# Performance work log

Measured on AMD Instinct MI355X. Metric: run time of the kernel, lower is better.

## Reference

```python
import jax, jax.numpy as jnp
import numpy as np

H = 16   # n_heads == n_I
D = 64   # d_q = d_k = d_v = d_r
DX = H * D
B, S = 4, 2048

def setup_inputs() -> dict:
    key = jax.random.key(0)
    ks = jax.random.split(key, 9)
    sc = 0.02
    return {
        "value": jax.random.normal(ks[0], (B, S, DX), jnp.float32),
        "key":   jax.random.normal(ks[1], (B, S, DX), jnp.float32),
        "query": jax.random.normal(ks[2], (B, S, DX), jnp.float32),
        "Wq_w": jax.random.normal(ks[3], (DX, DX), jnp.float32) * sc,
        "Wq_b": jnp.zeros((DX,), jnp.float32),
        "Wk_w": jax.random.normal(ks[4], (DX, DX), jnp.float32) * sc,
        "Wk_b": jnp.zeros((DX,), jnp.float32),
        "Wv_w": jax.random.normal(ks[5], (DX, DX), jnp.float32) * sc,
        "Wv_b": jnp.zeros((DX,), jnp.float32),
        "Wr_w": jax.random.normal(ks[6], (DX, DX), jnp.float32) * sc,
        "Wr_b": jnp.zeros((DX,), jnp.float32),
        "Wout_w": jax.random.normal(ks[7], (DX, DX), jnp.float32) * sc,
        "Wout_b": jnp.zeros((DX,), jnp.float32),
    }

def _heads(x, b, s):
    # [b, s, H*D] -> [b, H, s, D]
    return x.reshape(b, s, H, D).transpose(0, 2, 1, 3)

def reference(value, key, query, Wq_w, Wq_b, Wk_w, Wk_b, Wv_w, Wv_b,
              Wr_w, Wr_b, Wout_w, Wout_b):
    b, s, _ = query.shape
    # torch nn.Linear: y = x @ W.T + b
    Q = _heads(query @ Wq_w.T + Wq_b, b, s)   # [b,H,s,D]
    K = _heads(key   @ Wk_w.T + Wk_b, b, s)
    V = _heads(value @ Wv_w.T + Wv_b, b, s)
    R = _heads(query @ Wr_w.T + Wr_b, b, s)
    dot_scale = jnp.sqrt(jnp.float32(D))
    scores = jnp.einsum("bhid,bhjd->bhij", Q, K) / dot_scale  # [b,H,s,s]
    attn = jax.nn.softmax(scores, axis=-1)                    # dropout p=0
    out = jnp.einsum("bhij,bhjd->bhid", attn, V)              # [b,H,s,D]
    out = out * R                                             # R-gating
    out = out.transpose(0, 2, 1, 3).reshape(b, s, H * D)
    return out @ Wout_w.T + Wout_b
```

## Files before the change

kernel.cpp:

```cpp
#include <hip/hip_runtime.h>
#include <hip/hip_bf16.h>

typedef __bf16 bf16;
typedef __bf16 bf16x4 __attribute__((ext_vector_type(4)));
typedef __bf16 bf16x8 __attribute__((ext_vector_type(8)));
typedef float  f32x4  __attribute__((ext_vector_type(4)));

#define MFMA_16x16x32(a, b, c) __builtin_amdgcn_mfma_f32_16x16x32_bf16((a), (b), (c), 0, 0, 0)

typedef const void __attribute__((address_space(1))) gvoid;
typedef void __attribute__((address_space(3))) svoid;

__device__ __forceinline__ void async_copy16(const void* gptr, void* ldsptr) {
    __builtin_amdgcn_global_load_lds((gvoid*)gptr, (svoid*)ldsptr, 16, 0, 0);
}

__device__ __forceinline__ int swz8(int row, int quad) {
    return (quad ^ ((row >> 1) & 3)) * 8;
}

__global__ void cvt3_acts(const float* __restrict__ s0, const float* __restrict__ s1,
                          const float* __restrict__ s2,
                          bf16* __restrict__ d0, bf16* __restrict__ d1, bf16* __restrict__ d2)
{
    constexpr int N4SEG = 8192 * 1024 / 4;
    int i = blockIdx.x * blockDim.x + threadIdx.x;
    const int stride = gridDim.x * blockDim.x;
    for (; i < 3 * N4SEG; i += stride) {
        const int seg = i / N4SEG;
        const int j = i - seg * N4SEG;
        const float* s = seg == 0 ? s0 : (seg == 1 ? s1 : s2);
        bf16* d = seg == 0 ? d0 : (seg == 1 ? d1 : d2);
        float4 v = ((const float4*)s)[j];
        bf16x4 o = { (bf16)v.x, (bf16)v.y, (bf16)v.z, (bf16)v.w };
        ((bf16x4*)d)[j] = o;
    }
}

__global__ void cvt5_wts(const float* __restrict__ s0, const float* __restrict__ s1,
                         const float* __restrict__ s2, const float* __restrict__ s3,
                         const float* __restrict__ s4,
                         bf16* __restrict__ d0, bf16* __restrict__ d1, bf16* __restrict__ d2,
                         bf16* __restrict__ d3, bf16* __restrict__ d4)
{
    constexpr int N4SEG = 1024 * 1024 / 4;
    int i = blockIdx.x * blockDim.x + threadIdx.x;
    const int stride = gridDim.x * blockDim.x;
    for (; i < 5 * N4SEG; i += stride) {
        const int seg = i / N4SEG;
        const int j = i - seg * N4SEG;
        const float* s = seg == 0 ? s0 : seg == 1 ? s1 : seg == 2 ? s2 : seg == 3 ? s3 : s4;
        bf16* d = seg == 0 ? d0 : seg == 1 ? d1 : seg == 2 ? d2 : seg == 3 ? d3 : d4;
        float4 v = ((const float4*)s)[j];
        bf16x4 o = { (bf16)v.x, (bf16)v.y, (bf16)v.z, (bf16)v.w };
        ((bf16x4*)d)[j] = o;
    }
}

__global__ void proj_fused(const bf16* __restrict__ xq, const bf16* __restrict__ xk,
                           const bf16* __restrict__ xv, const bf16* __restrict__ wall,
                           const float* __restrict__ ball,
                           bf16* __restrict__ qr, bf16* __restrict__ kws,
                           bf16* __restrict__ vtws)
{
    constexpr int K = 1024, SDIM = 2048;
    __shared__ alignas(16) bf16 As[2][128 * 32];
    __shared__ alignas(16) bf16 Bs[2][128 * 32];

    const int tid  = threadIdx.x;
    const int lane = tid & 63;
    const int wave = tid >> 6;
    const int wm   = wave >> 1;
    const int wn   = wave & 1;
    const int bm   = blockIdx.x * 128;
    const int by   = blockIdx.y;
    const int bn   = by * 128;
    const int l15  = lane & 15;
    const int quad = lane >> 4;

    const bf16* X = (by < 16) ? xq : (by < 24 ? xk : xv);

    const int srow = lane >> 2;
    const int scol = (lane & 3) * 8;

    const bf16* aseg0 = X + (size_t)(bm + wave * 32 + srow) * K + scol;
    const bf16* aseg1 = X + (size_t)(bm + wave * 32 + 16 + srow) * K + scol;
    const bf16* bseg0 = wall + (size_t)(bn + wave * 32 + srow) * K + scol;
    const bf16* bseg1 = wall + (size_t)(bn + wave * 32 + 16 + srow) * K + scol;

    f32x4 acc[4][4] = {};

    {
        bf16* as0 = As[0] + (wave * 2 + 0) * 512;
        bf16* as1 = As[0] + (wave * 2 + 1) * 512;
        bf16* bs0 = Bs[0] + (wave * 2 + 0) * 512;
        bf16* bs1 = Bs[0] + (wave * 2 + 1) * 512;
        async_copy16(aseg0, as0);
        async_copy16(aseg1, as1);
        async_copy16(bseg0, bs0);
        async_copy16(bseg1, bs1);
    }

    for (int k0 = 0; k0 < K; k0 += 32) {
        const int cur = (k0 >> 5) & 1;
        __syncthreads();
        if (k0 + 32 < K) {
            const int nxt = cur ^ 1;
            async_copy16(aseg0 + k0 + 32, As[nxt] + (wave * 2 + 0) * 512);
            async_copy16(aseg1 + k0 + 32, As[nxt] + (wave * 2 + 1) * 512);
            async_copy16(bseg0 + k0 + 32, Bs[nxt] + (wave * 2 + 0) * 512);
            async_copy16(bseg1 + k0 + 32, Bs[nxt] + (wave * 2 + 1) * 512);
        }

        bf16x8 af[4], bfr[4];
        #pragma unroll
        for (int i = 0; i < 4; ++i)
            af[i] = *(const bf16x8*)(As[cur] + (wm * 64 + i * 16 + l15) * 32 + quad * 8);
        #pragma unroll
        for (int j = 0; j < 4; ++j)
            bfr[j] = *(const bf16x8*)(Bs[cur] + (wn * 64 + j * 16 + l15) * 32 + quad * 8);
        #pragma unroll
        for (int i = 0; i < 4; ++i)
            #pragma unroll
            for (int j = 0; j < 4; ++j)
                acc[i][j] = MFMA_16x16x32(af[i], bfr[j], acc[i][j]);
    }

    #pragma unroll
    for (int i = 0; i < 4; ++i) {
        const int rowg = bm + wm * 64 + i * 16 + quad * 4;
        #pragma unroll
        for (int j = 0; j < 4; ++j) {
            const int colg = bn + wn * 64 + j * 16 + l15;
            const float bv = ball[colg];
            if (by < 16) {
                #pragma unroll
                for (int r = 0; r < 4; ++r)
                    qr[(size_t)(rowg + r) * 2048 + colg] = (bf16)(acc[i][j][r] + bv);
            } else if (by < 24) {
                const int cl = colg - 2048;
                #pragma unroll
                for (int r = 0; r < 4; ++r)
                    kws[(size_t)(rowg + r) * 1024 + cl] = (bf16)(acc[i][j][r] + bv);
            } else {
                const int d = colg - 3072;
                bf16x4 o;
                #pragma unroll
                for (int r = 0; r < 4; ++r) o[r] = (bf16)(acc[i][j][r] + bv);
                *(bf16x4*)(vtws + (size_t)(rowg >> 11) * 1024 * SDIM
                                + (size_t)d * SDIM + (rowg & (SDIM - 1))) = o;
            }
        }
    }
}

__global__ void gemm_out(const bf16* __restrict__ X, const bf16* __restrict__ W,
                         const float* __restrict__ bias, float* __restrict__ Y)
{
    constexpr int K = 1024, N = 1024;
    __shared__ alignas(16) bf16 As[2][128 * 32];
    __shared__ alignas(16) bf16 Bs[2][128 * 32];

    const int tid  = threadIdx.x;
    const int lane = tid & 63;
    const int wave = tid >> 6;
    const int wm   = wave >> 1;
    const int wn   = wave & 1;
    const int bm   = blockIdx.x * 128;
    const int bn   = blockIdx.y * 128;
    const int l15  = lane & 15;
    const int quad = lane >> 4;

    const int srow = lane >> 2;
    const int scol = (lane & 3) * 8;

    const bf16* aseg0 = X + (size_t)(bm + wave * 32 + srow) * K + scol;
    const bf16* aseg1 = X + (size_t)(bm + wave * 32 + 16 + srow) * K + scol;
    const bf16* bseg0 = W + (size_t)(bn + wave * 32 + srow) * K + scol;
    const bf16* bseg1 = W + (size_t)(bn + wave * 32 + 16 + srow) * K + scol;

    f32x4 acc[4][4] = {};

    {
        async_copy16(aseg0, As[0] + (wave * 2 + 0) * 512);
        async_copy16(aseg1, As[0] + (wave * 2 + 1) * 512);
        async_copy16(bseg0, Bs[0] + (wave * 2 + 0) * 512);
        async_copy16(bseg1, Bs[0] + (wave * 2 + 1) * 512);
    }

    for (int k0 = 0; k0 < K; k0 += 32) {
        const int cur = (k0 >> 5) & 1;
        __syncthreads();
        if (k0 + 32 < K) {
            const int nxt = cur ^ 1;
            async_copy16(aseg0 + k0 + 32, As[nxt] + (wave * 2 + 0) * 512);
            async_copy16(aseg1 + k0 + 32, As[nxt] + (wave * 2 + 1) * 512);
            async_copy16(bseg0 + k0 + 32, Bs[nxt] + (wave * 2 + 0) * 512);
            async_copy16(bseg1 + k0 + 32, Bs[nxt] + (wave * 2 + 1) * 512);
        }

        bf16x8 af[4], bfr[4];
        #pragma unroll
        for (int i = 0; i < 4; ++i)
            af[i] = *(const bf16x8*)(As[cur] + (wm * 64 + i * 16 + l15) * 32 + quad * 8);
        #pragma unroll
        for (int j = 0; j < 4; ++j)
            bfr[j] = *(const bf16x8*)(Bs[cur] + (wn * 64 + j * 16 + l15) * 32 + quad * 8);
        #pragma unroll
        for (int i = 0; i < 4; ++i)
            #pragma unroll
            for (int j = 0; j < 4; ++j)
                acc[i][j] = MFMA_16x16x32(af[i], bfr[j], acc[i][j]);
    }

    #pragma unroll
    for (int i = 0; i < 4; ++i) {
        const int rowg = bm + wm * 64 + i * 16 + quad * 4;
        #pragma unroll
        for (int j = 0; j < 4; ++j) {
            const int colg = bn + wn * 64 + j * 16 + l15;
            const float bv = bias[colg];
            #pragma unroll
            for (int r = 0; r < 4; ++r)
                Y[(size_t)(rowg + r) * N + colg] = acc[i][j][r] + bv;
        }
    }
}

__launch_bounds__(256, 4)
__global__ void attn_fused(const bf16* __restrict__ QRp, const bf16* __restrict__ Kp,
                           const bf16* __restrict__ Vtp, bf16* __restrict__ Op)
{
    constexpr int S = 2048, DXc = 1024, QRST = 2048, Dh = 64;
    constexpr int PST = 40;
    __shared__ alignas(16) bf16 Ks[2][2][64 * 32];
    __shared__ alignas(16) bf16 Vt[2][2][64 * 32];
    __shared__ alignas(16) bf16 Pt[4][2][2][16 * PST];

    const int tid  = threadIdx.x;
    const int lane = tid & 63;
    const int wave = tid >> 6;
    const int qt = blockIdx.x, h = blockIdx.y, b = blockIdx.z;
    const int l15  = lane & 15;
    const int quad = lane >> 4;

    const size_t qrbase = ((size_t)b * S) * QRST + h * Dh;
    const size_t kbase  = ((size_t)b * S) * DXc + h * Dh;
    const size_t vtbase = ((size_t)(b * 16 + h) * Dh) * S;
    const size_t obase  = ((size_t)b * S) * DXc + h * Dh;

    const int srow = lane >> 2;
    const int scol = ((lane & 3) ^ ((srow >> 1) & 3)) * 8;
    const bf16* kseg = Kp  + kbase  + (size_t)(16 * wave + srow) * DXc + scol;
    const bf16* vseg = Vtp + vtbase + (size_t)(16 * wave + srow) * S   + scol;
    const int soff = wave * 512;

    async_copy16(kseg,      &Ks[0][0][soff]);
    async_copy16(kseg + 32, &Ks[0][1][soff]);
    async_copy16(vseg,      &Vt[0][0][soff]);
    async_copy16(vseg + 32, &Vt[0][1][soff]);

    constexpr float QSCALE = 0.125f * 1.44269504088896340736f;
    bf16x8 qf[2][2];
    #pragma unroll
    for (int mi = 0; mi < 2; ++mi) {
        const int qrow = qt * 128 + wave * 32 + mi * 16 + l15;
        const bf16* qptr = QRp + qrbase + (size_t)qrow * QRST + quad * 8;
        qf[mi][0] = *(const bf16x8*)(qptr);
        qf[mi][1] = *(const bf16x8*)(qptr + 32);
        #pragma unroll
        for (int j = 0; j < 8; ++j) {
            qf[mi][0][j] = (bf16)((float)qf[mi][0][j] * QSCALE);
            qf[mi][1][j] = (bf16)((float)qf[mi][1][j] * QSCALE);
        }
    }

    bf16x8 onef;
    #pragma unroll
    for (int j = 0; j < 8; ++j) onef[j] = (bf16)1.0f;

    f32x4 oacc[2][4] = {};
    f32x4 lsacc[2] = {};

    for (int t = 0; t < S / 64; ++t) {
        const int cur = t & 1;
        __syncthreads();
        if (t + 1 < S / 64) {
            const int nxt = cur ^ 1;
            const size_t ko = (size_t)(t + 1) * 64 * DXc;
            const int    vo = (t + 1) * 64;
            async_copy16(kseg + ko,      &Ks[nxt][0][soff]);
            async_copy16(kseg + ko + 32, &Ks[nxt][1][soff]);
            async_copy16(vseg + vo,      &Vt[nxt][0][soff]);
            async_copy16(vseg + vo + 32, &Vt[nxt][1][soff]);
        }

        f32x4 st[2][4];
        #pragma unroll
        for (int nb = 0; nb < 4; ++nb) {
            bf16x8 kf0 = *(const bf16x8*)(&Ks[cur][0][0] + (nb * 16 + l15) * 32 + swz8(l15, quad));
            bf16x8 kf1 = *(const bf16x8*)(&Ks[cur][1][0] + (nb * 16 + l15) * 32 + swz8(l15, quad));
            #pragma unroll
            for (int mi = 0; mi < 2; ++mi) {
                f32x4 z = {0.f, 0.f, 0.f, 0.f};
                z = MFMA_16x16x32(kf1, qf[mi][1], z);
                st[mi][nb] = MFMA_16x16x32(kf0, qf[mi][0], z);
            }
        }
        #pragma unroll
        for (int mi = 0; mi < 2; ++mi) {
            #pragma unroll
            for (int nb = 0; nb < 4; ++nb) {
                bf16x4 pt;
                #pragma unroll
                for (int r = 0; r < 4; ++r) {
                    float p = __builtin_exp2f(st[mi][nb][r]);
                    pt[r] = (bf16)p;
                }
                *(bf16x4*)(&Pt[wave][mi][nb >> 1][0] + l15 * PST
                           + (nb & 1) * 16 + quad * 4) = pt;
            }
        }

        #pragma unroll
        for (int half = 0; half < 2; ++half) {
            const bf16* vb = &Vt[cur][half][0];
            bf16x8 vtf[4];
            #pragma unroll
            for (int db = 0; db < 4; ++db)
                vtf[db] = *(const bf16x8*)(vb + (db * 16 + l15) * 32 + swz8(l15, quad));
            #pragma unroll
            for (int mi = 0; mi < 2; ++mi) {
                bf16x8 pf = *(const bf16x8*)(&Pt[wave][mi][half][0]
                                             + l15 * PST + quad * 8);
                #pragma unroll
                for (int db = 0; db < 4; ++db)
                    oacc[mi][db] = MFMA_16x16x32(vtf[db], pf, oacc[mi][db]);
                lsacc[mi] = MFMA_16x16x32(onef, pf, lsacc[mi]);
            }
        }
    }

    #pragma unroll
    for (int mi = 0; mi < 2; ++mi) {
        const float inv = 1.0f / lsacc[mi][0];
        const int qrow = qt * 128 + wave * 32 + mi * 16 + l15;
        const bf16* rrow = QRp + qrbase + (size_t)qrow * QRST + 1024;
        bf16* orow = Op + obase + (size_t)qrow * DXc;
        #pragma unroll
        for (int db = 0; db < 4; ++db) {
            bf16x4 rg = *(const bf16x4*)(rrow + db * 16 + quad * 4);
            bf16x4 o;
            #pragma unroll
            for (int r = 0; r < 4; ++r)
                o[r] = (bf16)(oacc[mi][db][r] * inv * (float)rg[r]);
            *(bf16x4*)(orow + db * 16 + quad * 4) = o;
        }
    }
}

extern "C" void kernel_launch(void* const* d_in, const int* in_sizes, int n_in,
                              void* d_out, int out_size, void* d_ws, size_t ws_size,
                              hipStream_t stream)
{
    (void)in_sizes; (void)n_in; (void)out_size; (void)ws_size;
    constexpr int B = 4, S = 2048, DX = 1024, M = B * S;
    constexpr size_t MD = (size_t)M * DX;
    constexpr size_t WD = (size_t)DX * DX;

    const float* value  = (const float*)d_in[0];
    const float* keyi   = (const float*)d_in[1];
    const float* query  = (const float*)d_in[2];
    const float* Wq_w   = (const float*)d_in[3];
    const float* Wq_b   = (const float*)d_in[4];
    const float* Wk_w   = (const float*)d_in[5];
    const float* Wk_b   = (const float*)d_in[6];
    const float* Wv_w   = (const float*)d_in[7];
    const float* Wv_b   = (const float*)d_in[8];
    const float* Wr_w   = (const float*)d_in[9];
    const float* Wr_b   = (const float*)d_in[10];
    const float* Wout_w = (const float*)d_in[11];
    const float* Wout_b = (const float*)d_in[12];

    bf16* p = (bf16*)d_ws;
    bf16* xv   = p;  p += MD;
    bf16* xk   = p;  p += MD;
    bf16* xq   = p;  p += MD;
    bf16* wall = p;  p += 4 * WD;
    bf16* wo   = p;  p += WD;
    bf16* qr   = p;  p += 2 * MD;
    bf16* kws  = p;  p += MD;
    bf16* vtws = p;  p += MD;
    float* ball = (float*)p;
    bf16* ows = xv;

    hipMemcpyAsync(ball,            Wq_b, DX * sizeof(float), hipMemcpyDeviceToDevice, stream);
    hipMemcpyAsync(ball + DX,       Wr_b, DX * sizeof(float), hipMemcpyDeviceToDevice, stream);
    hipMemcpyAsync(ball + 2 * DX,   Wk_b, DX * sizeof(float), hipMemcpyDeviceToDevice, stream);
    hipMemcpyAsync(ball + 3 * DX,   Wv_b, DX * sizeof(float), hipMemcpyDeviceToDevice, stream);

    cvt3_acts<<<dim3(2048), dim3(256), 0, stream>>>(value, keyi, query, xv, xk, xq);
    cvt5_wts <<<dim3(1024), dim3(256), 0, stream>>>(Wq_w, Wr_w, Wk_w, Wv_w, Wout_w,
                                                    wall, wall + WD, wall + 2 * WD,
                                                    wall + 3 * WD, wo);

    proj_fused<<<dim3(M / 128, 32), dim3(256), 0, stream>>>(
        xq, xk, xv, wall, ball, qr, kws, vtws);

    attn_fused<<<dim3(S / 128, 16, B), dim3(256), 0, stream>>>(qr, kws, vtws, ows);

    gemm_out<<<dim3(M / 128, DX / 128), dim3(256), 0, stream>>>(
        ows, wo, Wout_b, (float*)d_out);
}
```

Baseline: 410.4 us.

## Single-buffer attention K/V tiles and halve P scratch to raise occupancy

The attention kernel drops double buffering of K and V tiles and loads each tile synchronously, with barriers before and after the copy. The P scratch per wave is halved by interleaving the score/exp and PV steps per 32-key half. Launch bounds go from 4 to 6 blocks per CU. Together these cut LDS and register use so more blocks can be resident, at the cost of exposing global-load latency on every tile. The GEMM prologue edits are cosmetic.

```diff
diff --git a/kernel.cpp b/kernel.cpp
--- a/kernel.cpp
+++ b/kernel.cpp
@@ -90,16 +90,10 @@
 
     f32x4 acc[4][4] = {};
 
-    {
-        bf16* as0 = As[0] + (wave * 2 + 0) * 512;
-        bf16* as1 = As[0] + (wave * 2 + 1) * 512;
-        bf16* bs0 = Bs[0] + (wave * 2 + 0) * 512;
-        bf16* bs1 = Bs[0] + (wave * 2 + 1) * 512;
-        async_copy16(aseg0, as0);
-        async_copy16(aseg1, as1);
-        async_copy16(bseg0, bs0);
-        async_copy16(bseg1, bs1);
-    }
+    async_copy16(aseg0, As[0] + (wave * 2 + 0) * 512);
+    async_copy16(aseg1, As[0] + (wave * 2 + 1) * 512);
+    async_copy16(bseg0, Bs[0] + (wave * 2 + 0) * 512);
+    async_copy16(bseg1, Bs[0] + (wave * 2 + 1) * 512);
 
     for (int k0 = 0; k0 < K; k0 += 32) {
         const int cur = (k0 >> 5) & 1;
@@ -181,12 +175,10 @@
 
     f32x4 acc[4][4] = {};
 
-    {
-        async_copy16(aseg0, As[0] + (wave * 2 + 0) * 512);
-        async_copy16(aseg1, As[0] + (wave * 2 + 1) * 512);
-        async_copy16(bseg0, Bs[0] + (wave * 2 + 0) * 512);
-        async_copy16(bseg1, Bs[0] + (wave * 2 + 1) * 512);
-    }
+    async_copy16(aseg0, As[0] + (wave * 2 + 0) * 512);
+    async_copy16(aseg1, As[0] + (wave * 2 + 1) * 512);
+    async_copy16(bseg0, Bs[0] + (wave * 2 + 0) * 512);
+    async_copy16(bseg1, Bs[0] + (wave * 2 + 1) * 512);
 
     for (int k0 = 0; k0 < K; k0 += 32) {
         const int cur = (k0 >> 5) & 1;
@@ -227,15 +219,15 @@
     }
 }
 
-__launch_bounds__(256, 4)
+__launch_bounds__(256, 6)
 __global__ void attn_fused(const bf16* __restrict__ QRp, const bf16* __restrict__ Kp,
                            const bf16* __restrict__ Vtp, bf16* __restrict__ Op)
 {
     constexpr int S = 2048, DXc = 1024, QRST = 2048, Dh = 64;
     constexpr int PST = 40;
-    __shared__ alignas(16) bf16 Ks[2][2][64 * 32];
-    __shared__ alignas(16) bf16 Vt[2][2][64 * 32];
-    __shared__ alignas(16) bf16 Pt[4][2][2][16 * PST];
+    __shared__ alignas(16) bf16 Ks[2][64 * 32];
+    __shared__ alignas(16) bf16 Vt[2][64 * 32];
+    __shared__ alignas(16) bf16 Pt[4][2][16 * PST];
 
     const int tid  = threadIdx.x;
     const int lane = tid & 63;
@@ -249,90 +241,77 @@
     const size_t vtbase = ((size_t)(b * 16 + h) * Dh) * S;
     const size_t obase  = ((size_t)b * S) * DXc + h * Dh;
 
+    constexpr float QSCALE = 0.125f * 1.44269504088896340736f;
+    bf16x8 qf[2][2];
+    #pragma unroll
+    for (int mi = 0; mi < 2; ++mi) {
+        const int qrow = qt * 128 + wave * 32 + mi * 16 + l15;
+        const bf16* qptr = QRp + qrbase + (size_t)qrow * QRST + quad * 8;
+        qf[mi][0] = *(const bf16x8*)(qptr);
+        qf[mi][1] = *(const bf16x8*)(qptr + 32);
+        #pragma unroll
+        for (int j = 0; j < 8; ++j) {
+            qf[mi][0][j] = (bf16)((float)qf[mi][0][j] * QSCALE);
+            qf[mi][1][j] = (bf16)((float)qf[mi][1][j] * QSCALE);
+        }
+    }
+
+    bf16x8 onef;
+    #pragma unroll
+    for (int j = 0; j < 8; ++j) onef[j] = (bf16)1.0f;
+
+    f32x4 oacc[2][4] = {};
+    f32x4 lsacc[2] = {};
+
     const int srow = lane >> 2;
     const int scol = ((lane & 3) ^ ((srow >> 1) & 3)) * 8;
     const bf16* kseg = Kp  + kbase  + (size_t)(16 * wave + srow) * DXc + scol;
     const bf16* vseg = Vtp + vtbase + (size_t)(16 * wave + srow) * S   + scol;
     const int soff = wave * 512;
 
-    async_copy16(kseg,      &Ks[0][0][soff]);
-    async_copy16(kseg + 32, &Ks[0][1][soff]);
-    async_copy16(vseg,      &Vt[0][0][soff]);
-    async_copy16(vseg + 32, &Vt[0][1][soff]);
-
-    constexpr float QSCALE = 0.125f * 1.44269504088896340736f;
-    bf16x8 qf[2][2];
-    #pragma unroll
-    for (int mi = 0; mi < 2; ++mi) {
-        const int qrow = qt * 128 + wave * 32 + mi * 16 + l15;
-        const bf16* qptr = QRp + qrbase + (size_t)qrow * QRST + quad * 8;
-        qf[mi][0] = *(const bf16x8*)(qptr);
-        qf[mi][1] = *(const bf16x8*)(qptr + 32);
-        #pragma unroll
-        for (int j = 0; j < 8; ++j) {
-            qf[mi][0][j] = (bf16)((float)qf[mi][0][j] * QSCALE);
-            qf[mi][1][j] = (bf16)((float)qf[mi][1][j] * QSCALE);
-        }
-    }
-
-    bf16x8 onef;
-    #pragma unroll
-    for (int j = 0; j < 8; ++j) onef[j] = (bf16)1.0f;
-
-    f32x4 oacc[2][4] = {};
-    f32x4 lsacc[2] = {};
-
-    for (int t = 0; t < S / 64; ++t) {
-        const int cur = t & 1;
+    for (int kv0 = 0; kv0 < S; kv0 += 64) {
         __syncthreads();
-        if (t + 1 < S / 64) {
-            const int nxt = cur ^ 1;
-            const size_t ko = (size_t)(t + 1) * 64 * DXc;
-            const int    vo = (t + 1) * 64;
-            async_copy16(kseg + ko,      &Ks[nxt][0][soff]);
-            async_copy16(kseg + ko + 32, &Ks[nxt][1][soff]);
-            async_copy16(vseg + vo,      &Vt[nxt][0][soff]);
-            async_copy16(vseg + vo + 32, &Vt[nxt][1][soff]);
-        }
-
-        f32x4 st[2][4];
-        #pragma unroll
-        for (int nb = 0; nb < 4; ++nb) {
-            bf16x8 kf0 = *(const bf16x8*)(&Ks[cur][0][0] + (nb * 16 + l15) * 32 + swz8(l15, quad));
-            bf16x8 kf1 = *(const bf16x8*)(&Ks[cur][1][0] + (nb * 16 + l15) * 32 + swz8(l15, quad));
+        async_copy16(kseg + (size_t)kv0 * DXc,      &Ks[0][soff]);
+        async_copy16(kseg + (size_t)kv0 * DXc + 32, &Ks[1][soff]);
+        async_copy16(vseg + kv0,                    &Vt[0][soff]);
+        async_copy16(vseg + kv0 + 32,               &Vt[1][soff]);
+        __syncthreads();
+
+        #pragma unroll
+        for (int half = 0; half < 2; ++half) {
+            f32x4 st[2][2];
+            #pragma unroll
+            for (int nbl = 0; nbl < 2; ++nbl) {
+                const int nb = half * 2 + nbl;
+                bf16x8 kf0 = *(const bf16x8*)(&Ks[0][0] + (nb * 16 + l15) * 32 + swz8(l15, quad));
+                bf16x8 kf1 = *(const bf16x8*)(&Ks[1][0] + (nb * 16 + l15) * 32 + swz8(l15, quad));
+                #pragma unroll
+                for (int mi = 0; mi < 2; ++mi) {
+                    f32x4 z = {0.f, 0.f, 0.f, 0.f};
+                    z = MFMA_16x16x32(kf1, qf[mi][1], z);
+                    st[mi][nbl] = MFMA_16x16x32(kf0, qf[mi][0], z);
+                }
+            }
             #pragma unroll
             for (int mi = 0; mi < 2; ++mi) {
-                f32x4 z = {0.f, 0.f, 0.f, 0.f};
-                z = MFMA_16x16x32(kf1, qf[mi][1], z);
-                st[mi][nb] = MFMA_16x16x32(kf0, qf[mi][0], z);
+                #pragma unroll
+                for (int nbl = 0; nbl < 2; ++nbl) {
+                    bf16x4 pt;
+                    #pragma unroll
+                    for (int r = 0; r < 4; ++r)
+                        pt[r] = (bf16)__builtin_exp2f(st[mi][nbl][r]);
+                    *(bf16x4*)(&Pt[wave][mi][0] + l15 * PST
+                               + nbl * 16 + quad * 4) = pt;
+                }
             }
-        }
-        #pragma unroll
-        for (int mi = 0; mi < 2; ++mi) {
-            #pragma unroll
-            for (int nb = 0; nb < 4; ++nb) {
-                bf16x4 pt;
-                #pragma unroll
-                for (int r = 0; r < 4; ++r) {
-                    float p = __builtin_exp2f(st[mi][nb][r]);
-                    pt[r] = (bf16)p;
-                }
-                *(bf16x4*)(&Pt[wave][mi][nb >> 1][0] + l15 * PST
-                           + (nb & 1) * 16 + quad * 4) = pt;
-            }
-        }
-
-        #pragma unroll
-        for (int half = 0; half < 2; ++half) {
-            const bf16* vb = &Vt[cur][half][0];
+            const bf16* vb = &Vt[half][0];
             bf16x8 vtf[4];
             #pragma unroll
             for (int db = 0; db < 4; ++db)
                 vtf[db] = *(const bf16x8*)(vb + (db * 16 + l15) * 32 + swz8(l15, quad));
             #pragma unroll
             for (int mi = 0; mi < 2; ++mi) {
-                bf16x8 pf = *(const bf16x8*)(&Pt[wave][mi][half][0]
-                                             + l15 * PST + quad * 8);
+                bf16x8 pf = *(const bf16x8*)(&Pt[wave][mi][0] + l15 * PST + quad * 8);
                 #pragma unroll
                 for (int db = 0; db < 4; ++db)
                     oacc[mi][db] = MFMA_16x16x32(vtf[db], pf, oacc[mi][db]);
```

New measurement: 693.9 us. 1.69x slower.
